# Kernel tuning notes

Measured on AMD Instinct MI355X. Metric: run time of the kernel, lower is better.

Reference implementation:

```python
import jax, jax.numpy as jnp
import numpy as np

B, T, V, E, U = 8192, 1, 4000, 256, 256
IN = E + E  # GRU input dim: concat(features[B,1,256], embedded tokens[B,1,256]) -> 512


def setup_inputs() -> dict:
    key = jax.random.key(0)
    ks = jax.random.split(key, 8)
    s = 0.05
    return {
        "tokens": jax.random.randint(ks[0], (B, T), 0, V),
        "features": jax.random.normal(ks[1], (B, E), jnp.float32),
        "hidden": jnp.zeros((B, U), jnp.float32),  # unused by the original call (gru gets no initial_state)
        "emb": jax.random.normal(ks[2], (V, E), jnp.float32) * s,
        "gru_kernel": jax.random.normal(ks[3], (IN, 3 * U), jnp.float32) * s,
        "gru_rkernel": jax.random.normal(ks[4], (U, 3 * U), jnp.float32) * s,
        "gru_bias": jnp.zeros((2, 3 * U), jnp.float32),  # reset_after=True: separate input/recurrent biases
        "fc1_w": jax.random.normal(ks[5], (U, U), jnp.float32) * s,
        "fc1_b": jnp.zeros((U,), jnp.float32),
        "fc2_w": jax.random.normal(ks[6], (U, V), jnp.float32) * s,
        "fc2_b": jnp.zeros((V,), jnp.float32),
    }


def reference(tokens, features, hidden, emb, gru_kernel, gru_rkernel, gru_bias,
              fc1_w, fc1_b, fc2_w, fc2_b):
    # Embedding lookup: [B,T,E]
    x = emb[tokens]
    # concat context vector on feature axis (forces T==1): [B,1,E+E]
    x = jnp.concatenate([features[:, None, :], x], axis=-1)
    # Keras GRU called without initial_state -> zeros initial state.
    h0 = jnp.zeros((x.shape[0], U), x.dtype)

    def step(h, xt):  # xt: [B, IN]; Keras GRU v3 (reset_after=True) cell; dropout off at inference
        gx = xt @ gru_kernel + gru_bias[0]      # [B, 3U]
        gh = h @ gru_rkernel + gru_bias[1]      # [B, 3U]
        xz, xr, xn = jnp.split(gx, 3, axis=-1)
        hz, hr, hn = jnp.split(gh, 3, axis=-1)
        z = jax.nn.sigmoid(xz + hz)
        r = jax.nn.sigmoid(xr + hr)
        n = jnp.tanh(xn + r * hn)
        h_new = z * h + (1.0 - z) * n
        return h_new, h_new

    state, seq = jax.lax.scan(step, h0, jnp.swapaxes(x, 0, 1))  # seq: [T,B,U]
    out = jnp.swapaxes(seq, 0, 1)               # [B,T,U]
    y = out @ fc1_w + fc1_b                     # [B,T,U]
    y = y.reshape(-1, y.shape[-1])              # [B*T, U]
    logits = y @ fc2_w + fc2_b                  # [B*T, V]
    return (logits, state)
```

## Files before the change

### kernel.cpp

```cpp
#include <hip/hip_runtime.h>
#include <stdint.h>

typedef unsigned short u16;
typedef __attribute__((ext_vector_type(8))) short bf16x8;
typedef __attribute__((ext_vector_type(4))) float f32x4;

#define Bsz   8192
#define Vv    4000
#define Vpad  4096
#define Ee    256
#define Uu    256
#define INd   512
#define G3    768

__device__ __forceinline__ u16 f2bf(float f) {
    union { float f; uint32_t i; } v; v.f = f;
    uint32_t x = v.i;
    return (u16)((x + 0x7fffu + ((x >> 16) & 1u)) >> 16);
}

__device__ __forceinline__ void gload16(const u16* g, u16* l) {
    __builtin_amdgcn_global_load_lds(
        (const __attribute__((address_space(1))) unsigned int*)g,
        (__attribute__((address_space(3))) unsigned int*)l, 16, 0, 0);
}

__global__ __launch_bounds__(256) void prep_w1(
    const float* __restrict__ w1, u16* __restrict__ w1t)
{
    __shared__ float t[32][33];
    int b  = blockIdx.x;
    int bx = b % 24, by = b / 24;
    int n0 = bx * 32, k0 = by * 32;
    int c = threadIdx.x & 31, r = threadIdx.x >> 5;
    #pragma unroll
    for (int i = 0; i < 32; i += 8)
        t[r + i][c] = w1[(size_t)(k0 + r + i) * 768 + n0 + c];
    __syncthreads();
    #pragma unroll
    for (int i = 0; i < 32; i += 8)
        w1t[(size_t)(n0 + r + i) * 512 + k0 + c] = f2bf(t[c][r + i]);
}

__global__ __launch_bounds__(256) void mid_all(
    const int* __restrict__ tokens, const float* __restrict__ features,
    const float* __restrict__ emb,  const u16* __restrict__ BT,
    const float* __restrict__ gb,
    u16* __restrict__ h,
    float* __restrict__ state,
    const float* __restrict__ fc2,
    const float* __restrict__ fc1,
    const float* __restrict__ fc1b, const float* __restrict__ fc2b,
    u16* __restrict__ Wt,
    float* __restrict__ bfused)
{
    __shared__ __align__(16) char smem[33024];
    int b   = blockIdx.x;
    int tid = threadIdx.x;

    if (b < 512) {
        u16* AsP = (u16*)smem;
        u16* BsP = AsP + 4096;
        int* tok = (int*)(smem + 32768);

        int sid = (b & 7) * 64 + (b >> 3);
        int m0  = (sid >> 2) * 64;
        int n0  = (sid & 3) * 64;
        if (tid < 64) tok[tid] = tokens[m0 + tid];

        int wid = tid >> 6, lane = tid & 63, quad = lane >> 4, l16 = lane & 15;
        int wm = wid * 16;

        f32x4 acc[3][4] = {};

        int r  = tid >> 2;
        int kc = (tid & 3) * 8;
        const u16* bg = BT + (size_t)(n0 + r) * INd + kc;
        const float* fsrc = features + (size_t)(m0 + r) * Ee + kc;

        #pragma unroll
        for (int g = 0; g < 3; g++)
            gload16(bg + (size_t)g * 256 * INd, &BsP[g * 2048 + tid * 8]);
        float4 a = *(const float4*)fsrc;
        float4 c = *(const float4*)(fsrc + 4);
        {
            u16 o[8] = {f2bf(a.x), f2bf(a.y), f2bf(a.z), f2bf(a.w),
                        f2bf(c.x), f2bf(c.y), f2bf(c.z), f2bf(c.w)};
            *(uint4*)&AsP[tid * 8] = *(const uint4*)o;
        }
        a = *(const float4*)(fsrc + 32);
        c = *(const float4*)(fsrc + 36);

        int cur = 0;
        for (int k0 = 0; k0 < INd; k0 += 32) {
            __syncthreads();
            int k1 = k0 + 32;
            if (k1 < INd) {
                #pragma unroll
                for (int g = 0; g < 3; g++)
                    gload16(bg + (size_t)g * 256 * INd + k1,
                            &BsP[(cur ^ 1) * 6144 + g * 2048 + tid * 8]);
                u16 o[8] = {f2bf(a.x), f2bf(a.y), f2bf(a.z), f2bf(a.w),
                            f2bf(c.x), f2bf(c.y), f2bf(c.z), f2bf(c.w)};
                *(uint4*)&AsP[(cur ^ 1) * 2048 + tid * 8] = *(const uint4*)o;
                int k2 = k0 + 64;
                if (k2 < INd) {
                    const float* src = (k2 < Ee) ? (fsrc + k2)
                                     : (emb + (size_t)tok[r] * Ee + (k2 - Ee) + kc);
                    a = *(const float4*)src;
                    c = *(const float4*)(src + 4);
                }
            }
            bf16x8 af = *(const bf16x8*)&AsP[cur * 2048 + (wm + l16) * 32 + quad * 8];
            #pragma unroll
            for (int g = 0; g < 3; g++)
                #pragma unroll
                for (int j = 0; j < 4; j++) {
                    bf16x8 bfv = *(const bf16x8*)&BsP[cur * 6144 + g * 2048
                                                     + (j * 16 + l16) * 32 + quad * 8];
                    acc[g][j] = __builtin_amdgcn_mfma_f32_16x16x32_bf16(af, bfv, acc[g][j], 0, 0, 0);
                }
            cur ^= 1;
        }

        #pragma unroll
        for (int j = 0; j < 4; j++) {
            int jj = n0 + j * 16 + l16;
            float bz  = gb[jj]          + gb[G3 + jj];
            float br  = gb[Uu + jj]     + gb[G3 + Uu + jj];
            float b0n = gb[2 * Uu + jj];
            float b1n = gb[G3 + 2 * Uu + jj];
            #pragma unroll
            for (int rr = 0; rr < 4; rr++) {
                int bb = m0 + wm + quad * 4 + rr;
                float z  = 1.f / (1.f + __expf(-(acc[0][j][rr] + bz)));
                float rg = 1.f / (1.f + __expf(-(acc[1][j][rr] + br)));
                float n  = tanhf(acc[2][j][rr] + b0n + rg * b1n);
                float hv = (1.f - z) * n;
                h[(size_t)bb * Uu + jj] = f2bf(hv);
                state[(size_t)bb * Uu + jj] = hv;
            }
        }
    } else if (b < 768) {
        int wb = b - 512;
        int i0 = (wb & 3) * 64;
        int n0 = (wb >> 2) * 64;
        u16* Aw = (u16*)smem;
        u16* Bw = Aw + 2048;

        int wid = tid >> 6, lane = tid & 63, quad = lane >> 4, l16 = lane & 15;
        int wm  = wid * 16;
        int nn  = tid >> 2, jc = (tid & 3) * 8;
        int nv  = n0 + nn;
        bool nok = nv < Vv;

        f32x4 acc[4] = {};
        float a8[8]; float4 bA, bB;

        #define WT_LOAD(J0)                                                        \
            do {                                                                   \
                _Pragma("unroll")                                                  \
                for (int p = 0; p < 8; p++)                                        \
                    a8[p] = nok ? fc2[(size_t)((J0) + jc + p) * Vv + nv] : 0.f;    \
                bA = *(const float4*)&fc1[(size_t)(i0 + nn) * 256 + (J0) + jc];    \
                bB = *(const float4*)&fc1[(size_t)(i0 + nn) * 256 + (J0) + jc + 4];\
            } while (0)

        WT_LOAD(0);
        for (int t = 0; t < 8; t++) {
            __syncthreads();
            {
                u16 oa[8] = {f2bf(a8[0]), f2bf(a8[1]), f2bf(a8[2]), f2bf(a8[3]),
                             f2bf(a8[4]), f2bf(a8[5]), f2bf(a8[6]), f2bf(a8[7])};
                *(uint4*)&Aw[tid * 8] = *(const uint4*)oa;
                u16 ob[8] = {f2bf(bA.x), f2bf(bA.y), f2bf(bA.z), f2bf(bA.w),
                             f2bf(bB.x), f2bf(bB.y), f2bf(bB.z), f2bf(bB.w)};
                *(uint4*)&Bw[tid * 8] = *(const uint4*)ob;
            }
            __syncthreads();
            if (t < 7) WT_LOAD((t + 1) * 32);
            bf16x8 af = *(const bf16x8*)&Aw[(wm + l16) * 32 + quad * 8];
            #pragma unroll
            for (int j = 0; j < 4; j++) {
                bf16x8 bfv = *(const bf16x8*)&Bw[(j * 16 + l16) * 32 + quad * 8];
                acc[j] = __builtin_amdgcn_mfma_f32_16x16x32_bf16(af, bfv, acc[j], 0, 0, 0);
            }
        }
        #undef WT_LOAD

        #pragma unroll
        for (int j = 0; j < 4; j++)
            #pragma unroll
            for (int rr = 0; rr < 4; rr++)
                Wt[(size_t)(n0 + wm + quad * 4 + rr) * 256 + i0 + j * 16 + l16]
                    = f2bf(acc[j][rr]);
    } else {
        float* red = (float*)smem;
        int bb = b - 768;
        int nl = bb * 64 + (tid & 63);
        int kq = tid >> 6;
        float s = 0.f;
        if (nl < Vv) {
            #pragma unroll 8
            for (int k = 0; k < 64; k++) {
                int kk = kq * 64 + k;
                s += fc1b[kk] * fc2[(size_t)kk * Vv + nl];
            }
        }
        red[kq * 64 + (tid & 63)] = s;
        __syncthreads();
        if (kq == 0 && nl < Vv)
            bfused[nl] = red[nl & 63] + red[64 + (nl & 63)] + red[128 + (nl & 63)]
                       + red[192 + (nl & 63)] + fc2b[nl];
    }
}

template<int BMt, int BNt, bool OUT_BF16, bool HAS_BIAS>
__global__ __launch_bounds__(256) void gemm_bt(
    const u16* __restrict__ A, const u16* __restrict__ BT,
    const float* __restrict__ bias, void* __restrict__ Cout,
    int N, int K)
{
    constexpr int NW_N  = (BNt == 128) ? 2 : 1;
    constexpr int NW_M  = 4 / NW_N;
    constexpr int WROWS = BMt / NW_M;
    constexpr int MI    = WROWS / 16;

    __shared__ __align__(16) u16 As[2][BMt * 32];
    __shared__ __align__(16) u16 Bs[2][BNt * 32];

    int tid = threadIdx.x;
    int m0   = blockIdx.y * BMt;
    int n0   = blockIdx.x * BNt;
    int wid  = tid >> 6, lane = tid & 63, quad = lane >> 4, l16 = lane & 15;
    int wm   = (wid / NW_N) * WROWS;
    int wn   = (wid % NW_N) * 64;

    f32x4 acc[MI][4] = {};

    const u16* ag = A  + (size_t)(m0 + (tid >> 2)) * K + (tid & 3) * 8;
    const u16* bg = BT + (size_t)(n0 + (tid >> 2)) * K + (tid & 3) * 8;

    #pragma unroll
    for (int s = 0; s < BMt / 64; s++)
        gload16(ag + (size_t)s * 64 * K, &As[0][tid * 8 + s * 64 * 32]);
    #pragma unroll
    for (int s = 0; s < BNt / 64; s++)
        gload16(bg + (size_t)s * 64 * K, &Bs[0][tid * 8 + s * 64 * 32]);

    int cur = 0;
    for (int k0 = 0; k0 < K; k0 += 32) {
        __syncthreads();
        int k1 = k0 + 32;
        if (k1 < K) {
            #pragma unroll
            for (int s = 0; s < BMt / 64; s++)
                gload16(ag + (size_t)s * 64 * K + k1, &As[cur ^ 1][tid * 8 + s * 64 * 32]);
            #pragma unroll
            for (int s = 0; s < BNt / 64; s++)
                gload16(bg + (size_t)s * 64 * K + k1, &Bs[cur ^ 1][tid * 8 + s * 64 * 32]);
        }

        bf16x8 af[MI], bf[4];
        #pragma unroll
        for (int i = 0; i < MI; i++)
            af[i] = *(const bf16x8*)&As[cur][(wm + i * 16 + l16) * 32 + quad * 8];
        #pragma unroll
        for (int j = 0; j < 4; j++)
            bf[j] = *(const bf16x8*)&Bs[cur][(wn + j * 16 + l16) * 32 + quad * 8];
        #pragma unroll
        for (int i = 0; i < MI; i++)
            #pragma unroll
            for (int j = 0; j < 4; j++)
                acc[i][j] = __builtin_amdgcn_mfma_f32_16x16x32_bf16(af[i], bf[j], acc[i][j], 0, 0, 0);
        cur ^= 1;
    }

    #pragma unroll
    for (int i = 0; i < MI; i++)
    #pragma unroll
    for (int j = 0; j < 4; j++) {
        int gn = n0 + wn + j * 16 + l16;
        if (gn >= N) continue;
        float bv = HAS_BIAS ? bias[gn] : 0.f;
        #pragma unroll
        for (int r = 0; r < 4; r++) {
            int gm = m0 + wm + i * 16 + quad * 4 + r;
            float v = acc[i][j][r] + bv;
            if (OUT_BF16) ((u16*)Cout)[(size_t)gm * N + gn] = f2bf(v);
            else          ((float*)Cout)[(size_t)gm * N + gn] = v;
        }
    }
}

extern "C" void kernel_launch(void* const* d_in, const int* in_sizes, int n_in,
                              void* d_out, int out_size, void* d_ws, size_t ws_size,
                              hipStream_t stream)
{
    const int*   tokens   = (const int*)d_in[0];
    const float* features = (const float*)d_in[1];
    const float* emb      = (const float*)d_in[3];
    const float* w1       = (const float*)d_in[4];
    const float* gbias    = (const float*)d_in[6];
    const float* fc1w     = (const float*)d_in[7];
    const float* fc1b     = (const float*)d_in[8];
    const float* fc2w     = (const float*)d_in[9];
    const float* fc2b     = (const float*)d_in[10];

    float* logits = (float*)d_out;
    float* state  = logits + (size_t)Bsz * Vv;

    char* ws = (char*)d_ws;
    u16*   w1t    = (u16*)(ws);
    u16*   Wt     = (u16*)(ws +   786432);
    u16*   h      = (u16*)(ws +  2883584);
    float* bfused = (float*)(ws +  7077888);

    prep_w1<<<dim3(384), 256, 0, stream>>>(w1, w1t);

    mid_all<<<dim3(832), 256, 0, stream>>>(
        tokens, features, emb, w1t, gbias, h, state,
        fc2w, fc1w, fc1b, fc2b, Wt, bfused);

    gemm_bt<128, 128, false, true><<<dim3(Vpad / 128, Bsz / 128), 256, 0, stream>>>(
        h, Wt, bfused, (void*)logits, Vv, Uu);
}
```

Measured before the change: 211.4 us.

## Merge weight prep and GRU stage into one cooperative kernel with grid sync

Result: slower. 357.9 us (+69.3%).

```diff
diff --git a/kernel.cpp b/kernel.cpp
--- a/kernel.cpp
+++ b/kernel.cpp
@@ -1,5 +1,8 @@
 #include <hip/hip_runtime.h>
+#include <hip/hip_cooperative_groups.h>
 #include <stdint.h>
+
+namespace cg = cooperative_groups;
 
 typedef unsigned short u16;
 typedef __attribute__((ext_vector_type(8))) short bf16x8;
@@ -25,40 +28,58 @@
         (__attribute__((address_space(3))) unsigned int*)l, 16, 0, 0);
 }
 
-__global__ __launch_bounds__(256) void prep_w1(
-    const float* __restrict__ w1, u16* __restrict__ w1t)
-{
-    __shared__ float t[32][33];
-    int b  = blockIdx.x;
-    int bx = b % 24, by = b / 24;
-    int n0 = bx * 32, k0 = by * 32;
-    int c = threadIdx.x & 31, r = threadIdx.x >> 5;
-    #pragma unroll
-    for (int i = 0; i < 32; i += 8)
-        t[r + i][c] = w1[(size_t)(k0 + r + i) * 768 + n0 + c];
-    __syncthreads();
-    #pragma unroll
-    for (int i = 0; i < 32; i += 8)
-        w1t[(size_t)(n0 + r + i) * 512 + k0 + c] = f2bf(t[c][r + i]);
-}
-
-__global__ __launch_bounds__(256) void mid_all(
+__global__ __launch_bounds__(256, 2) void front_all(
     const int* __restrict__ tokens, const float* __restrict__ features,
-    const float* __restrict__ emb,  const u16* __restrict__ BT,
+    const float* __restrict__ emb,  const float* __restrict__ w1,
     const float* __restrict__ gb,
+    const float* __restrict__ fc1,  const float* __restrict__ fc1b,
+    const float* __restrict__ fc2,  const float* __restrict__ fc2b,
+    u16* __restrict__ w1t,
+    u16* __restrict__ Wt,
     u16* __restrict__ h,
     float* __restrict__ state,
-    const float* __restrict__ fc2,
-    const float* __restrict__ fc1,
-    const float* __restrict__ fc1b, const float* __restrict__ fc2b,
-    u16* __restrict__ Wt,
     float* __restrict__ bfused)
 {
     __shared__ __align__(16) char smem[33024];
     int b   = blockIdx.x;
     int tid = threadIdx.x;
 
-    if (b < 512) {
+    if (b < 384) {
+        float (*t)[33] = (float(*)[33])smem;
+        int bx = b % 24, by = b / 24;
+        int n0 = bx * 32, k0 = by * 32;
+        int c = tid & 31, r = tid >> 5;
+        #pragma unroll
+        for (int i = 0; i < 32; i += 8)
+            t[r + i][c] = w1[(size_t)(k0 + r + i) * 768 + n0 + c];
+        __syncthreads();
+        #pragma unroll
+        for (int i = 0; i < 32; i += 8)
+            w1t[(size_t)(n0 + r + i) * 512 + k0 + c] = f2bf(t[c][r + i]);
+    } else if (b < 448) {
+        float* red = (float*)smem;
+        int bb = b - 384;
+        int nl = bb * 64 + (tid & 63);
+        int kq = tid >> 6;
+        float s = 0.f;
+        if (nl < Vv) {
+            #pragma unroll 8
+            for (int k = 0; k < 64; k++) {
+                int kk = kq * 64 + k;
+                s += fc1b[kk] * fc2[(size_t)kk * Vv + nl];
+            }
+        }
+        red[kq * 64 + (tid & 63)] = s;
+        __syncthreads();
+        if (kq == 0 && nl < Vv)
+            bfused[nl] = red[nl & 63] + red[64 + (nl & 63)] + red[128 + (nl & 63)]
+                       + red[192 + (nl & 63)] + fc2b[nl];
+    }
+
+    __threadfence();
+    cg::this_grid().sync();
+
+    {
         u16* AsP = (u16*)smem;
         u16* BsP = AsP + 4096;
         int* tok = (int*)(smem + 32768);
@@ -66,6 +87,7 @@
         int sid = (b & 7) * 64 + (b >> 3);
         int m0  = (sid >> 2) * 64;
         int n0  = (sid & 3) * 64;
+        __syncthreads();
         if (tid < 64) tok[tid] = tokens[m0 + tid];
 
         int wid = tid >> 6, lane = tid & 63, quad = lane >> 4, l16 = lane & 15;
@@ -75,7 +97,7 @@
 
         int r  = tid >> 2;
         int kc = (tid & 3) * 8;
-        const u16* bg = BT + (size_t)(n0 + r) * INd + kc;
+        const u16* bg = w1t + (size_t)(n0 + r) * INd + kc;
         const float* fsrc = features + (size_t)(m0 + r) * Ee + kc;
 
         #pragma unroll
@@ -141,10 +163,11 @@
                 state[(size_t)bb * Uu + jj] = hv;
             }
         }
-    } else if (b < 768) {
-        int wb = b - 512;
-        int i0 = (wb & 3) * 64;
-        int n0 = (wb >> 2) * 64;
+    }
+
+    if (b < 256) {
+        int i0 = (b & 3) * 64;
+        int n0 = (b >> 2) * 64;
         u16* Aw = (u16*)smem;
         u16* Bw = Aw + 2048;
 
@@ -194,24 +217,6 @@
             for (int rr = 0; rr < 4; rr++)
                 Wt[(size_t)(n0 + wm + quad * 4 + rr) * 256 + i0 + j * 16 + l16]
                     = f2bf(acc[j][rr]);
-    } else {
-        float* red = (float*)smem;
-        int bb = b - 768;
-        int nl = bb * 64 + (tid & 63);
-        int kq = tid >> 6;
-        float s = 0.f;
-        if (nl < Vv) {
-            #pragma unroll 8
-            for (int k = 0; k < 64; k++) {
-                int kk = kq * 64 + k;
-                s += fc1b[kk] * fc2[(size_t)kk * Vv + nl];
-            }
-        }
-        red[kq * 64 + (tid & 63)] = s;
-        __syncthreads();
-        if (kq == 0 && nl < Vv)
-            bfused[nl] = red[nl & 63] + red[64 + (nl & 63)] + red[128 + (nl & 63)]
-                       + red[192 + (nl & 63)] + fc2b[nl];
     }
 }
 
@@ -316,11 +321,12 @@
     u16*   h      = (u16*)(ws +  2883584);
     float* bfused = (float*)(ws +  7077888);
 
-    prep_w1<<<dim3(384), 256, 0, stream>>>(w1, w1t);
-
-    mid_all<<<dim3(832), 256, 0, stream>>>(
-        tokens, features, emb, w1t, gbias, h, state,
-        fc2w, fc1w, fc1b, fc2b, Wt, bfused);
+    void* args[] = {
+        (void*)&tokens, (void*)&features, (void*)&emb, (void*)&w1, (void*)&gbias,
+        (void*)&fc1w, (void*)&fc1b, (void*)&fc2w, (void*)&fc2b,
+        (void*)&w1t, (void*)&Wt, (void*)&h, (void*)&state, (void*)&bfused
+    };
+    hipLaunchCooperativeKernel((void*)front_all, dim3(512), dim3(256), args, 0, stream);
 
     gemm_bt<128, 128, false, true><<<dim3(Vpad / 128, Bsz / 128), 256, 0, stream>>>(
         h, Wt, bfused, (void*)logits, Vv, Uu);
```
